# Kernel tuning notes

Measured on AMD Instinct MI355X. Metric: run time of the kernel, lower is better.

Reference implementation:

```python
import jax, jax.numpy as jnp
import numpy as np

N_USERS = 60000
N_ITEMS = 40000
N_NODES = N_USERS + N_ITEMS  # 100000
N_EDGES = 3_200_000
EMB_DIM = 64
N_LAYERS = 3
S_TEMP = 1.0  # config['s_temp']
EPS = 1e-16   # torch_geometric.utils.softmax denominator eps


def segment_softmax(logits, seg, num_segments):
    # numerically stable scatter-softmax (PyG softmax semantics)
    m = jax.ops.segment_max(logits, seg, num_segments=num_segments)
    m = jnp.where(jnp.isfinite(m), m, 0.0)  # empty segments -> -inf guard
    e = jnp.exp(logits - m[seg])
    s = jax.ops.segment_sum(e, seg, num_segments=num_segments)
    return e / (s[seg] + EPS)


def setup_inputs() -> dict:
    key = jax.random.key(0)
    k1, k2, k3 = jax.random.split(key, 3)
    # nn.Embedding weight, init normal(std=0.1) for non-NGCF models
    emb = jax.random.normal(k1, (N_NODES, EMB_DIM), dtype=jnp.float32) * 0.1
    edge_index = jax.random.randint(k2, (2, N_EDGES), 0, N_NODES, dtype=jnp.int32)
    edge_attrs = jax.random.normal(k3, (N_EDGES,), dtype=jnp.float32)
    return {"emb": emb, "edge_index": edge_index, "edge_attrs": edge_attrs}


def reference(emb, edge_index, edge_attrs):
    from_, to_ = edge_index[0], edge_index[1]
    logits = edge_attrs / S_TEMP
    incoming = segment_softmax(logits, to_, N_NODES)
    outgoing = segment_softmax(logits, from_, N_NODES)
    norm = jnp.sqrt(incoming * outgoing)  # abl_study == 0 branch

    embs = [emb]
    cur = emb
    for _ in range(N_LAYERS):
        # message: norm * x_j ; aggregate: scatter-add at to_
        msg = norm[:, None] * cur[from_]           # [E, D]
        cur = jax.ops.segment_sum(msg, to_, num_segments=N_NODES)  # [N, D]
        embs.append(cur)

    out = jnp.mean(jnp.stack(embs, axis=0), axis=0)  # lightGCN-style layer mean
    return (emb, out)
```

## Files before the change

### kernel.cpp

```cpp
#include <hip/hip_runtime.h>
#include <math.h>
#include <hip/hip_fp16.h>

#define N_NODES 100000
#define N_EDGES 3200000
#define EPS 1e-16f
#define BSH 8
#define BN 256
#define NBK 391
#define PTT 512
#define PE2 8
#define PTILE (PTT * PE2)
#define GR (PTILE / 16)
#define PBLOCKS ((N_EDGES + PTILE - 1) / PTILE)
#define CAP 9216u

typedef float    f4v __attribute__((ext_vector_type(4)));
typedef float    f2v __attribute__((ext_vector_type(2)));

static __device__ __forceinline__ float4 nt_load_f4(const float4* p) {
    f4v v = __builtin_nontemporal_load((const f4v*)p);
    return make_float4(v.x, v.y, v.z, v.w);
}

static __device__ __forceinline__ unsigned short f_to_bf(float f) {
    unsigned u = __float_as_uint(f);
    unsigned r = (u + 0x7FFFu + ((u >> 16) & 1u)) >> 16;
    return (unsigned short)r;
}
static __device__ __forceinline__ float slot_w(unsigned s) {
    return __half2float(__ushort_as_half((unsigned short)(s >> 17)));
}
static __device__ __forceinline__ void fma8(float w, uint4 r, float* a) {
    a[0] = fmaf(w, __uint_as_float(r.x << 16), a[0]);
    a[1] = fmaf(w, __uint_as_float(r.x & 0xFFFF0000u), a[1]);
    a[2] = fmaf(w, __uint_as_float(r.y << 16), a[2]);
    a[3] = fmaf(w, __uint_as_float(r.y & 0xFFFF0000u), a[3]);
    a[4] = fmaf(w, __uint_as_float(r.z << 16), a[4]);
    a[5] = fmaf(w, __uint_as_float(r.z & 0xFFFF0000u), a[5]);
    a[6] = fmaf(w, __uint_as_float(r.w << 16), a[6]);
    a[7] = fmaf(w, __uint_as_float(r.w & 0xFFFF0000u), a[7]);
}
static __device__ __forceinline__ void fma8_fp8(float w, uint2 r, float* a) {
    f2v v0 = __builtin_amdgcn_cvt_pk_f32_fp8((int)r.x, false);
    f2v v1 = __builtin_amdgcn_cvt_pk_f32_fp8((int)r.x, true);
    f2v v2 = __builtin_amdgcn_cvt_pk_f32_fp8((int)r.y, false);
    f2v v3 = __builtin_amdgcn_cvt_pk_f32_fp8((int)r.y, true);
    a[0] = fmaf(w, v0.x, a[0]); a[1] = fmaf(w, v0.y, a[1]);
    a[2] = fmaf(w, v1.x, a[2]); a[3] = fmaf(w, v1.y, a[3]);
    a[4] = fmaf(w, v2.x, a[4]); a[5] = fmaf(w, v2.y, a[5]);
    a[6] = fmaf(w, v3.x, a[6]); a[7] = fmaf(w, v3.y, a[7]);
}
static __device__ __forceinline__ uint4 pack8(const float* a) {
    uint4 o;
    o.x = (unsigned)f_to_bf(a[0]) | ((unsigned)f_to_bf(a[1]) << 16);
    o.y = (unsigned)f_to_bf(a[2]) | ((unsigned)f_to_bf(a[3]) << 16);
    o.z = (unsigned)f_to_bf(a[4]) | ((unsigned)f_to_bf(a[5]) << 16);
    o.w = (unsigned)f_to_bf(a[6]) | ((unsigned)f_to_bf(a[7]) << 16);
    return o;
}
static __device__ __forceinline__ uint2 pack8_fp8(const float* a) {
    int w0 = __builtin_amdgcn_cvt_pk_fp8_f32(a[0], a[1], 0, false);
    w0 = __builtin_amdgcn_cvt_pk_fp8_f32(a[2], a[3], w0, true);
    int w1 = __builtin_amdgcn_cvt_pk_fp8_f32(a[4], a[5], 0, false);
    w1 = __builtin_amdgcn_cvt_pk_fp8_f32(a[6], a[7], w1, true);
    return make_uint2((unsigned)w0, (unsigned)w1);
}
static __device__ __forceinline__ float bfu_to_f(unsigned u, int hi) {
    return __uint_as_float(hi ? (u & 0xFFFF0000u) : (u << 16));
}

__global__ __launch_bounds__(PTT) void partition(
        const int* __restrict__ ei, const float* __restrict__ attr,
        unsigned* __restrict__ pos_t, unsigned* __restrict__ pos_f,
        uint2* __restrict__ bt, unsigned* __restrict__ bf,
        const float4* __restrict__ emb4, float4* __restrict__ out_emb4,
        uint4* __restrict__ emb_bf) {
    __shared__ unsigned ht[NBK], hf[NBK];
    __shared__ unsigned hbt[NBK + 1], hbf[NBK + 1];
    __shared__ unsigned dlt[NBK], dlf[NBK];
    __shared__ unsigned short lutT[GR], lutF[GR];
    __shared__ unsigned wsum[8];
    __shared__ unsigned sbtx[PTILE], sbty[PTILE];
    __shared__ unsigned sbf[PTILE];
    const int tid = threadIdx.x;
    const int lane = tid & 63, wid = tid >> 6;
    for (int i = tid; i < NBK; i += PTT) { ht[i] = 0; hf[i] = 0; }
    __syncthreads();
    const int tile = blockIdx.x * PTILE;
    const int tcount = (tile + PTILE < N_EDGES) ? PTILE : (N_EDGES - tile);
    unsigned fv[PE2], tv[PE2];
    float xv[PE2];
    #pragma unroll
    for (int k = 0; k < PE2; ++k) {
        int e = tile + k * PTT + tid;
        if (e < N_EDGES) {
            fv[k] = (unsigned)__builtin_nontemporal_load(&ei[e]);
            tv[k] = (unsigned)__builtin_nontemporal_load(&ei[N_EDGES + e]);
            xv[k] = __expf(__builtin_nontemporal_load(&attr[e]));
            atomicAdd(&ht[tv[k] >> BSH], 1u);
            atomicAdd(&hf[fv[k] >> BSH], 1u);
        } else {
            tv[k] = 0xFFFFFFFFu;
        }
    }
    __syncthreads();
    unsigned ot = (tid < NBK) ? ht[tid] : 0u;
    unsigned of = (tid < NBK) ? hf[tid] : 0u;
    unsigned own = ot | (of << 16);
    unsigned x = own;
    #pragma unroll
    for (int d = 1; d < 64; d <<= 1) {
        unsigned v = __shfl_up(x, d, 64);
        if (lane >= d) x += v;
    }
    if (lane == 63) wsum[wid] = x;
    __syncthreads();
    unsigned pre = 0;
    for (int w = 0; w < wid; ++w) pre += wsum[w];
    unsigned excl = x + pre - own;
    unsigned et = excl & 0xFFFFu, ef = excl >> 16;
    if (tid < NBK) {
        hbt[tid] = et;
        hbf[tid] = ef;
        unsigned rt = ot ? atomicAdd(&pos_t[tid], ot) : 0u;
        unsigned rf = of ? atomicAdd(&pos_f[tid], of) : 0u;
        dlt[tid] = tid * CAP + rt - et;
        dlf[tid] = tid * CAP + rf - ef;
    }
    if (tid == NBK - 1) { hbt[NBK] = et + ot; hbf[NBK] = ef + of; }
    __syncthreads();
    if (tid < NBK) {
        unsigned b0 = hbt[tid], b1 = hbt[tid + 1];
        for (unsigned g = (b0 + 15u) >> 4; (g << 4) < b1; ++g) lutT[g] = (unsigned short)tid;
        b0 = hbf[tid]; b1 = hbf[tid + 1];
        for (unsigned g = (b0 + 15u) >> 4; (g << 4) < b1; ++g) lutF[g] = (unsigned short)tid;
    }
    for (int i = tid; i < NBK; i += PTT) { ht[i] = hbt[i]; hf[i] = hbf[i]; }
    __syncthreads();
    #pragma unroll
    for (int k = 0; k < PE2; ++k) {
        if (tv[k] != 0xFFFFFFFFu) {
            unsigned p = atomicAdd(&ht[tv[k] >> BSH], 1u);
            sbtx[p] = fv[k] | ((tv[k] & (BN - 1u)) << 17);
            sbty[p] = __float_as_uint(xv[k]);
            unsigned q = atomicAdd(&hf[fv[k] >> BSH], 1u);
            sbf[q] = ((fv[k] & (BN - 1u)) << 16) |
                     (unsigned)__half_as_ushort(__float2half(xv[k]));
        }
    }
    __syncthreads();
    for (int i = tid; i < tcount; i += PTT) {
        unsigned b = lutT[i >> 4];
        while (hbt[b + 1] <= (unsigned)i) ++b;
        unsigned ga = dlt[b] + (unsigned)i;
        if (ga < (b + 1u) * CAP) bt[ga] = make_uint2(sbtx[i], sbty[i]);
    }
    for (int i = tid; i < tcount; i += PTT) {
        unsigned b = lutF[i >> 4];
        while (hbf[b + 1] <= (unsigned)i) ++b;
        unsigned ga = dlf[b] + (unsigned)i;
        if (ga < (b + 1u) * CAP) bf[ga] = sbf[i];
    }
    for (int i = blockIdx.x * PTT + tid; i < N_NODES * 8; i += PBLOCKS * PTT) {
        float4 v0 = nt_load_f4(&emb4[2 * i]);
        float4 v1 = nt_load_f4(&emb4[2 * i + 1]);
        out_emb4[2 * i] = v0;
        out_emb4[2 * i + 1] = v1;
        float a[8] = {v0.x, v0.y, v0.z, v0.w, v1.x, v1.y, v1.z, v1.w};
        emb_bf[i] = pack8(a);
    }
}

__global__ __launch_bounds__(512) void bucket_sum_f(
        const unsigned* __restrict__ pos_f, const unsigned* __restrict__ bf,
        float* __restrict__ s_from_inv) {
    __shared__ float s[BN];
    int b = blockIdx.x, tid = threadIdx.x;
    if (tid < BN) s[tid] = 0.f;
    __syncthreads();
    unsigned fill = pos_f[b]; if (fill > CAP) fill = CAP;
    unsigned lo = b * CAP, hi = lo + fill;
    for (unsigned i = lo + tid; i < hi; i += 512) {
        unsigned u = __builtin_nontemporal_load(&bf[i]);
        atomicAdd(&s[u >> 16], __half2float(__ushort_as_half((unsigned short)(u & 0xFFFFu))));
    }
    __syncthreads();
    if (tid < BN) {
        int node = b * BN + tid;
        if (node < N_NODES) s_from_inv[node] = rsqrtf(s[tid] + EPS);
    }
}

__global__ __launch_bounds__(512) void bucket_csr_t(
        const unsigned* __restrict__ pos_t, const uint2* __restrict__ bt,
        const float* __restrict__ s_from_inv,
        uint2* __restrict__ row2, unsigned* __restrict__ slots) {
    __shared__ unsigned cnt[BN];
    __shared__ float sto[BN];
    __shared__ float rs[BN];
    __shared__ unsigned cur[BN];
    __shared__ unsigned wsum[8];
    int b = blockIdx.x, tid = threadIdx.x;
    const int lane = tid & 63, wid = tid >> 6;
    if (tid < BN) { cnt[tid] = 0; sto[tid] = 0.f; }
    __syncthreads();
    unsigned fill = pos_t[b]; if (fill > CAP) fill = CAP;
    unsigned lo = b * CAP, hi = lo + fill;
    for (unsigned i = lo + tid; i < hi; i += 512) {
        uint2 u = bt[i];
        unsigned tl = u.x >> 17;
        atomicAdd(&cnt[tl], 1u);
        atomicAdd(&sto[tl], __uint_as_float(u.y));
    }
    __syncthreads();
    unsigned own = (tid < BN) ? cnt[tid] : 0u;
    unsigned x = own;
    #pragma unroll
    for (int d = 1; d < 64; d <<= 1) {
        unsigned v = __shfl_up(x, d, 64);
        if (lane >= d) x += v;
    }
    if (lane == 63) wsum[wid] = x;
    __syncthreads();
    unsigned pre = 0;
    for (int w = 0; w < wid; ++w) pre += wsum[w];
    unsigned excl = x + pre - own;
    if (tid < BN) {
        int node = b * BN + tid;
        if (node < N_NODES) row2[node] = make_uint2(lo + excl, lo + excl + own);
        rs[tid] = rsqrtf(sto[tid] + EPS);
        cur[tid] = lo + excl;
    }
    __syncthreads();
    for (unsigned i = lo + tid; i < hi; i += 512) {
        uint2 u = bt[i];
        unsigned tl = u.x >> 17;
        unsigned f = u.x & 0x1FFFFu;
        float w = __uint_as_float(u.y) * rs[tl] * s_from_inv[f];
        unsigned hb = (unsigned)__half_as_ushort(__float2half(w));
        unsigned p = atomicAdd(&cur[tl], 1u);
        slots[p] = f | (hb << 17);
    }
}

#define GATHER_CORE(TABLE)                                                        \
    float a[8] = {0, 0, 0, 0, 0, 0, 0, 0};                                        \
    float bacc[8] = {0, 0, 0, 0, 0, 0, 0, 0};                                     \
    unsigned k = beg;                                                             \
    for (; k + 8 <= end; k += 8) {                                                \
        unsigned s0 = slots[k], s1 = slots[k + 1], s2 = slots[k + 2], s3 = slots[k + 3]; \
        unsigned s4 = slots[k + 4], s5 = slots[k + 5], s6 = slots[k + 6], s7 = slots[k + 7]; \
        uint4 r0 = TABLE[(size_t)(s0 & 0x1FFFFu) * 8 + lane];                     \
        uint4 r1 = TABLE[(size_t)(s1 & 0x1FFFFu) * 8 + lane];                     \
        uint4 r2 = TABLE[(size_t)(s2 & 0x1FFFFu) * 8 + lane];                     \
        uint4 r3 = TABLE[(size_t)(s3 & 0x1FFFFu) * 8 + lane];                     \
        uint4 r4 = TABLE[(size_t)(s4 & 0x1FFFFu) * 8 + lane];                     \
        uint4 r5 = TABLE[(size_t)(s5 & 0x1FFFFu) * 8 + lane];                     \
        uint4 r6 = TABLE[(size_t)(s6 & 0x1FFFFu) * 8 + lane];                     \
        uint4 r7 = TABLE[(size_t)(s7 & 0x1FFFFu) * 8 + lane];                     \
        fma8(slot_w(s0), r0, a);    fma8(slot_w(s1), r1, bacc);                   \
        fma8(slot_w(s2), r2, a);    fma8(slot_w(s3), r3, bacc);                   \
        fma8(slot_w(s4), r4, a);    fma8(slot_w(s5), r5, bacc);                   \
        fma8(slot_w(s6), r6, a);    fma8(slot_w(s7), r7, bacc);                   \
    }                                                                             \
    for (; k < end; ++k) {                                                        \
        unsigned s = slots[k];                                                    \
        uint4 r = TABLE[(size_t)(s & 0x1FFFFu) * 8 + lane];                       \
        fma8(slot_w(s), r, a);                                                    \
    }                                                                             \
    _Pragma("unroll")                                                             \
    for (int j = 0; j < 8; ++j) a[j] += bacc[j];

#define GATHER_CORE8(TABLE)                                                       \
    float a[8] = {0, 0, 0, 0, 0, 0, 0, 0};                                        \
    float bacc[8] = {0, 0, 0, 0, 0, 0, 0, 0};                                     \
    unsigned k = beg;                                                             \
    for (; k + 8 <= end; k += 8) {                                                \
        unsigned s0 = slots[k], s1 = slots[k + 1], s2 = slots[k + 2], s3 = slots[k + 3]; \
        unsigned s4 = slots[k + 4], s5 = slots[k + 5], s6 = slots[k + 6], s7 = slots[k + 7]; \
        uint2 r0 = TABLE[(size_t)(s0 & 0x1FFFFu) * 8 + lane];                     \
        uint2 r1 = TABLE[(size_t)(s1 & 0x1FFFFu) * 8 + lane];                     \
        uint2 r2 = TABLE[(size_t)(s2 & 0x1FFFFu) * 8 + lane];                     \
        uint2 r3 = TABLE[(size_t)(s3 & 0x1FFFFu) * 8 + lane];                     \
        uint2 r4 = TABLE[(size_t)(s4 & 0x1FFFFu) * 8 + lane];                     \
        uint2 r5 = TABLE[(size_t)(s5 & 0x1FFFFu) * 8 + lane];                     \
        uint2 r6 = TABLE[(size_t)(s6 & 0x1FFFFu) * 8 + lane];                     \
        uint2 r7 = TABLE[(size_t)(s7 & 0x1FFFFu) * 8 + lane];                     \
        fma8_fp8(slot_w(s0), r0, a);    fma8_fp8(slot_w(s1), r1, bacc);           \
        fma8_fp8(slot_w(s2), r2, a);    fma8_fp8(slot_w(s3), r3, bacc);           \
        fma8_fp8(slot_w(s4), r4, a);    fma8_fp8(slot_w(s5), r5, bacc);           \
        fma8_fp8(slot_w(s6), r6, a);    fma8_fp8(slot_w(s7), r7, bacc);           \
    }                                                                             \
    for (; k < end; ++k) {                                                        \
        unsigned s = slots[k];                                                    \
        uint2 r = TABLE[(size_t)(s & 0x1FFFFu) * 8 + lane];                       \
        fma8_fp8(slot_w(s), r, a);                                                \
    }                                                                             \
    _Pragma("unroll")                                                             \
    for (int j = 0; j < 8; ++j) a[j] += bacc[j];

__global__ void prop1(const uint2* __restrict__ row2, const unsigned* __restrict__ slots,
                      const uint4* __restrict__ emb_bf,
                      uint2* __restrict__ T1f8, uint4* __restrict__ T1bf) {
    int node = blockIdx.x * 32 + (threadIdx.x >> 3);
    int lane = threadIdx.x & 7;
    if (node >= N_NODES) return;
    uint2 rp = row2[node];
    unsigned beg = rp.x, end = rp.y;
    GATHER_CORE(emb_bf)
    size_t o = (size_t)node * 8 + lane;
    T1bf[o] = pack8(a);
    T1f8[o] = pack8_fp8(a);
}

__global__ void prop2(const uint2* __restrict__ row2, const unsigned* __restrict__ slots,
                      const uint2* __restrict__ T1f8,
                      uint2* __restrict__ T2f8, uint4* __restrict__ T2bf) {
    int node = blockIdx.x * 32 + (threadIdx.x >> 3);
    int lane = threadIdx.x & 7;
    if (node >= N_NODES) return;
    uint2 rp = row2[node];
    unsigned beg = rp.x, end = rp.y;
    GATHER_CORE8(T1f8)
    size_t o = (size_t)node * 8 + lane;
    T2bf[o] = pack8(a);
    T2f8[o] = pack8_fp8(a);
}

__global__ void prop3(const uint2* __restrict__ row2, const unsigned* __restrict__ slots,
                      const uint2* __restrict__ T2f8,
                      const uint4* __restrict__ T1bf, const uint4* __restrict__ T2bf,
                      const float4* __restrict__ emb4, float4* __restrict__ acc) {
    int node = blockIdx.x * 32 + (threadIdx.x >> 3);
    int lane = threadIdx.x & 7;
    if (node >= N_NODES) return;
    uint2 rp = row2[node];
    unsigned beg = rp.x, end = rp.y;
    GATHER_CORE8(T2f8)
    size_t o = (size_t)node * 8 + lane;
    uint4 t1 = T1bf[o];
    uint4 t2 = T2bf[o];
    unsigned tw1[4] = {t1.x, t1.y, t1.z, t1.w};
    unsigned tw2[4] = {t2.x, t2.y, t2.z, t2.w};
    size_t o4 = (size_t)node * 16 + lane * 2;
    float4 e0 = emb4[o4], e1 = emb4[o4 + 1];
    float e[8] = {e0.x, e0.y, e0.z, e0.w, e1.x, e1.y, e1.z, e1.w};
    float r[8];
    #pragma unroll
    for (int j = 0; j < 8; ++j) {
        float l1v = bfu_to_f(tw1[j >> 1], j & 1);
        float l2v = bfu_to_f(tw2[j >> 1], j & 1);
        r[j] = (e[j] + l1v + l2v + a[j]) * 0.25f;
    }
    acc[o4]     = make_float4(r[0], r[1], r[2], r[3]);
    acc[o4 + 1] = make_float4(r[4], r[5], r[6], r[7]);
}

extern "C" void kernel_launch(void* const* d_in, const int* in_sizes, int n_in,
                              void* d_out, int out_size, void* d_ws, size_t ws_size,
                              hipStream_t stream) {
    const float* emb = (const float*)d_in[0];
    const int* ei = (const int*)d_in[1];
    const float* attr = (const float*)d_in[2];

    float* out_emb = (float*)d_out;
    float* out_acc = out_emb + (size_t)N_NODES * 64;

    char* ws = (char*)d_ws;
    size_t off = 0;
    auto alloc = [&](size_t bytes) -> void* {
        void* p = ws + off;
        off += (bytes + 255) & ~(size_t)255;
        return p;
    };
    unsigned* pos_t   = (unsigned*)alloc((size_t)NBK * 4);
    unsigned* pos_f   = (unsigned*)alloc((size_t)NBK * 4);
    size_t zero_bytes = off;
    uint2*    row2    = (uint2*)   alloc((size_t)N_NODES * 8);
    float* s_from_inv = (float*)   alloc((size_t)N_NODES * 4);
    uint2* bt         = (uint2*)   alloc((size_t)NBK * CAP * 8);
    unsigned* bfa     = (unsigned*)alloc((size_t)NBK * CAP * 4);
    unsigned* slots   = bfa;
    uint4* emb_bf     = (uint4*)   alloc((size_t)N_NODES * 128);
    uint2* T1f8       = (uint2*)   alloc((size_t)N_NODES * 64);
    uint4* T1bf       = (uint4*)   alloc((size_t)N_NODES * 128);
    uint2* T2f8 = (uint2*)bt;
    uint4* T2bf = (uint4*)((char*)bt + (size_t)N_NODES * 64);
    (void)ws_size;

    hipMemsetAsync(d_ws, 0, zero_bytes, stream);

    partition<<<PBLOCKS, PTT, 0, stream>>>(ei, attr, pos_t, pos_f, bt, bfa,
                                           (const float4*)emb, (float4*)out_emb, emb_bf);
    bucket_sum_f<<<NBK, 512, 0, stream>>>(pos_f, bfa, s_from_inv);
    bucket_csr_t<<<NBK, 512, 0, stream>>>(pos_t, bt, s_from_inv, row2, slots);

    const int pgrid = (N_NODES * 8 + 255) / 256;
    prop1<<<pgrid, 256, 0, stream>>>(row2, slots, emb_bf, T1f8, T1bf);
    prop2<<<pgrid, 256, 0, stream>>>(row2, slots, T1f8, T2f8, T2bf);
    prop3<<<pgrid, 256, 0, stream>>>(row2, slots, T2f8, T1bf, T2bf, (const float4*)emb,
                                     (float4*)out_acc);
}
```

Measured before the change: 279.5 us.

## Use fp8 embedding table for layer one, split CSR by source half, move emb copy

The first propagation layer now gathers from an fp8 copy of the input embeddings instead of bf16, halving gathered bytes per edge. The CSR builder orders each destination's edges so that sources below node 50000 come before the rest, aiming for better cache locality during gathers. The fp32 passthrough copy of emb to the output moves from the partition kernel into prop1, taking it off the partition kernel's path. The trade-off is lower precision in layer one, which may raise output error.

Result: faster. 270.6 us (-3.2%).

```diff
diff --git a/kernel.cpp b/kernel.cpp
--- a/kernel.cpp
+++ b/kernel.cpp
@@ -14,6 +14,7 @@
 #define GR (PTILE / 16)
 #define PBLOCKS ((N_EDGES + PTILE - 1) / PTILE)
 #define CAP 9216u
+#define FSPLIT 50000u
 
 typedef float    f4v __attribute__((ext_vector_type(4)));
 typedef float    f2v __attribute__((ext_vector_type(2)));
@@ -30,16 +31,6 @@
 }
 static __device__ __forceinline__ float slot_w(unsigned s) {
     return __half2float(__ushort_as_half((unsigned short)(s >> 17)));
-}
-static __device__ __forceinline__ void fma8(float w, uint4 r, float* a) {
-    a[0] = fmaf(w, __uint_as_float(r.x << 16), a[0]);
-    a[1] = fmaf(w, __uint_as_float(r.x & 0xFFFF0000u), a[1]);
-    a[2] = fmaf(w, __uint_as_float(r.y << 16), a[2]);
-    a[3] = fmaf(w, __uint_as_float(r.y & 0xFFFF0000u), a[3]);
-    a[4] = fmaf(w, __uint_as_float(r.z << 16), a[4]);
-    a[5] = fmaf(w, __uint_as_float(r.z & 0xFFFF0000u), a[5]);
-    a[6] = fmaf(w, __uint_as_float(r.w << 16), a[6]);
-    a[7] = fmaf(w, __uint_as_float(r.w & 0xFFFF0000u), a[7]);
 }
 static __device__ __forceinline__ void fma8_fp8(float w, uint2 r, float* a) {
     f2v v0 = __builtin_amdgcn_cvt_pk_f32_fp8((int)r.x, false);
@@ -74,8 +65,7 @@
         const int* __restrict__ ei, const float* __restrict__ attr,
         unsigned* __restrict__ pos_t, unsigned* __restrict__ pos_f,
         uint2* __restrict__ bt, unsigned* __restrict__ bf,
-        const float4* __restrict__ emb4, float4* __restrict__ out_emb4,
-        uint4* __restrict__ emb_bf) {
+        const float4* __restrict__ emb4, uint2* __restrict__ emb_f8) {
     __shared__ unsigned ht[NBK], hf[NBK];
     __shared__ unsigned hbt[NBK + 1], hbf[NBK + 1];
     __shared__ unsigned dlt[NBK], dlf[NBK];
@@ -165,10 +155,8 @@
     for (int i = blockIdx.x * PTT + tid; i < N_NODES * 8; i += PBLOCKS * PTT) {
         float4 v0 = nt_load_f4(&emb4[2 * i]);
         float4 v1 = nt_load_f4(&emb4[2 * i + 1]);
-        out_emb4[2 * i] = v0;
-        out_emb4[2 * i + 1] = v1;
         float a[8] = {v0.x, v0.y, v0.z, v0.w, v1.x, v1.y, v1.z, v1.w};
-        emb_bf[i] = pack8(a);
+        emb_f8[i] = pack8_fp8(a);
     }
 }
 
@@ -196,25 +184,28 @@
         const unsigned* __restrict__ pos_t, const uint2* __restrict__ bt,
         const float* __restrict__ s_from_inv,
         uint2* __restrict__ row2, unsigned* __restrict__ slots) {
-    __shared__ unsigned cnt[BN];
+    __shared__ unsigned cntL[BN], cntH[BN];
     __shared__ float sto[BN];
     __shared__ float rs[BN];
-    __shared__ unsigned cur[BN];
+    __shared__ unsigned curL[BN], curH[BN];
     __shared__ unsigned wsum[8];
     int b = blockIdx.x, tid = threadIdx.x;
     const int lane = tid & 63, wid = tid >> 6;
-    if (tid < BN) { cnt[tid] = 0; sto[tid] = 0.f; }
+    if (tid < BN) { cntL[tid] = 0; cntH[tid] = 0; sto[tid] = 0.f; }
     __syncthreads();
     unsigned fill = pos_t[b]; if (fill > CAP) fill = CAP;
     unsigned lo = b * CAP, hi = lo + fill;
     for (unsigned i = lo + tid; i < hi; i += 512) {
         uint2 u = bt[i];
         unsigned tl = u.x >> 17;
-        atomicAdd(&cnt[tl], 1u);
+        unsigned f = u.x & 0x1FFFFu;
+        atomicAdd((f < FSPLIT) ? &cntL[tl] : &cntH[tl], 1u);
         atomicAdd(&sto[tl], __uint_as_float(u.y));
     }
     __syncthreads();
-    unsigned own = (tid < BN) ? cnt[tid] : 0u;
+    unsigned ol = (tid < BN) ? cntL[tid] : 0u;
+    unsigned oh = (tid < BN) ? cntH[tid] : 0u;
+    unsigned own = ol + oh;
     unsigned x = own;
     #pragma unroll
     for (int d = 1; d < 64; d <<= 1) {
@@ -230,7 +221,8 @@
         int node = b * BN + tid;
         if (node < N_NODES) row2[node] = make_uint2(lo + excl, lo + excl + own);
         rs[tid] = rsqrtf(sto[tid] + EPS);
-        cur[tid] = lo + excl;
+        curL[tid] = lo + excl;
+        curH[tid] = lo + excl + ol;
     }
     __syncthreads();
     for (unsigned i = lo + tid; i < hi; i += 512) {
@@ -239,38 +231,10 @@
         unsigned f = u.x & 0x1FFFFu;
         float w = __uint_as_float(u.y) * rs[tl] * s_from_inv[f];
         unsigned hb = (unsigned)__half_as_ushort(__float2half(w));
-        unsigned p = atomicAdd(&cur[tl], 1u);
+        unsigned p = atomicAdd((f < FSPLIT) ? &curL[tl] : &curH[tl], 1u);
         slots[p] = f | (hb << 17);
     }
 }
-
-#define GATHER_CORE(TABLE)                                                        \
-    float a[8] = {0, 0, 0, 0, 0, 0, 0, 0};                                        \
-    float bacc[8] = {0, 0, 0, 0, 0, 0, 0, 0};                                     \
-    unsigned k = beg;                                                             \
-    for (; k + 8 <= end; k += 8) {                                                \
-        unsigned s0 = slots[k], s1 = slots[k + 1], s2 = slots[k + 2], s3 = slots[k + 3]; \
-        unsigned s4 = slots[k + 4], s5 = slots[k + 5], s6 = slots[k + 6], s7 = slots[k + 7]; \
-        uint4 r0 = TABLE[(size_t)(s0 & 0x1FFFFu) * 8 + lane];                     \
-        uint4 r1 = TABLE[(size_t)(s1 & 0x1FFFFu) * 8 + lane];                     \
-        uint4 r2 = TABLE[(size_t)(s2 & 0x1FFFFu) * 8 + lane];                     \
-        uint4 r3 = TABLE[(size_t)(s3 & 0x1FFFFu) * 8 + lane];                     \
-        uint4 r4 = TABLE[(size_t)(s4 & 0x1FFFFu) * 8 + lane];                     \
-        uint4 r5 = TABLE[(size_t)(s5 & 0x1FFFFu) * 8 + lane];                     \
-        uint4 r6 = TABLE[(size_t)(s6 & 0x1FFFFu) * 8 + lane];                     \
-        uint4 r7 = TABLE[(size_t)(s7 & 0x1FFFFu) * 8 + lane];                     \
-        fma8(slot_w(s0), r0, a);    fma8(slot_w(s1), r1, bacc);                   \
-        fma8(slot_w(s2), r2, a);    fma8(slot_w(s3), r3, bacc);                   \
-        fma8(slot_w(s4), r4, a);    fma8(slot_w(s5), r5, bacc);                   \
-        fma8(slot_w(s6), r6, a);    fma8(slot_w(s7), r7, bacc);                   \
-    }                                                                             \
-    for (; k < end; ++k) {                                                        \
-        unsigned s = slots[k];                                                    \
-        uint4 r = TABLE[(size_t)(s & 0x1FFFFu) * 8 + lane];                       \
-        fma8(slot_w(s), r, a);                                                    \
-    }                                                                             \
-    _Pragma("unroll")                                                             \
-    for (int j = 0; j < 8; ++j) a[j] += bacc[j];
 
 #define GATHER_CORE8(TABLE)                                                       \
     float a[8] = {0, 0, 0, 0, 0, 0, 0, 0};                                        \
@@ -301,17 +265,24 @@
     for (int j = 0; j < 8; ++j) a[j] += bacc[j];
 
 __global__ void prop1(const uint2* __restrict__ row2, const unsigned* __restrict__ slots,
-                      const uint4* __restrict__ emb_bf,
-                      uint2* __restrict__ T1f8, uint4* __restrict__ T1bf) {
+                      const uint2* __restrict__ emb_f8,
+                      uint2* __restrict__ T1f8, uint4* __restrict__ T1bf,
+                      const float4* __restrict__ emb4, float4* __restrict__ out_emb4) {
     int node = blockIdx.x * 32 + (threadIdx.x >> 3);
     int lane = threadIdx.x & 7;
-    if (node >= N_NODES) return;
-    uint2 rp = row2[node];
-    unsigned beg = rp.x, end = rp.y;
-    GATHER_CORE(emb_bf)
-    size_t o = (size_t)node * 8 + lane;
-    T1bf[o] = pack8(a);
-    T1f8[o] = pack8_fp8(a);
+    if (node < N_NODES) {
+        uint2 rp = row2[node];
+        unsigned beg = rp.x, end = rp.y;
+        GATHER_CORE8(emb_f8)
+        size_t o = (size_t)node * 8 + lane;
+        T1bf[o] = pack8(a);
+        T1f8[o] = pack8_fp8(a);
+    }
+    const int total = N_NODES * 16;
+    const int stride = ((N_NODES * 8 + 255) / 256) * 256;
+    for (int i = blockIdx.x * 256 + threadIdx.x; i < total; i += stride) {
+        out_emb4[i] = nt_load_f4(&emb4[i]);
+    }
 }
 
 __global__ void prop2(const uint2* __restrict__ row2, const unsigned* __restrict__ slots,
@@ -382,7 +353,7 @@
     uint2* bt         = (uint2*)   alloc((size_t)NBK * CAP * 8);
     unsigned* bfa     = (unsigned*)alloc((size_t)NBK * CAP * 4);
     unsigned* slots   = bfa;
-    uint4* emb_bf     = (uint4*)   alloc((size_t)N_NODES * 128);
+    uint2* emb_f8     = (uint2*)   alloc((size_t)N_NODES * 64);
     uint2* T1f8       = (uint2*)   alloc((size_t)N_NODES * 64);
     uint4* T1bf       = (uint4*)   alloc((size_t)N_NODES * 128);
     uint2* T2f8 = (uint2*)bt;
@@ -392,12 +363,13 @@
     hipMemsetAsync(d_ws, 0, zero_bytes, stream);
 
     partition<<<PBLOCKS, PTT, 0, stream>>>(ei, attr, pos_t, pos_f, bt, bfa,
-                                           (const float4*)emb, (float4*)out_emb, emb_bf);
+                                           (const float4*)emb, emb_f8);
     bucket_sum_f<<<NBK, 512, 0, stream>>>(pos_f, bfa, s_from_inv);
     bucket_csr_t<<<NBK, 512, 0, stream>>>(pos_t, bt, s_from_inv, row2, slots);
 
     const int pgrid = (N_NODES * 8 + 255) / 256;
-    prop1<<<pgrid, 256, 0, stream>>>(row2, slots, emb_bf, T1f8, T1bf);
+    prop1<<<pgrid, 256, 0, stream>>>(row2, slots, emb_f8, T1f8, T1bf,
+                                     (const float4*)emb, (float4*)out_emb);
     prop2<<<pgrid, 256, 0, stream>>>(row2, slots, T1f8, T2f8, T2bf);
     prop3<<<pgrid, 256, 0, stream>>>(row2, slots, T2f8, T1bf, T2bf, (const float4*)emb,
                                      (float4*)out_acc);
```
